# Kernel optimization log

Hardware: AMD Instinct MI355X
Metric: run time of the kernel (lower is better)

Reference implementation:

```python
import jax, jax.numpy as jnp
import numpy as np

B, T = 32, 1000
NN, NB, CTX = 512, 16, 64
EMB = 256
DCAT = 3 * EMB
H, L = 256, 4
PN, PB = 512, 2
S, V = 8, 64


def setup_inputs() -> dict:
    key = jax.random.key(0)
    ks = jax.random.split(key, 20)
    r = lambda i, shape, sc=1.0: jax.random.normal(ks[i], shape, dtype=jnp.float32) * sc
    nu_log = jnp.log(-jnp.log(jax.random.uniform(ks[8], (L, H), minval=0.5, maxval=0.95)))
    inp = {
        'neural_input': r(0, (B, T, NN)),
        'behavior_input': r(1, (B, T, NB)),
        'session_id': jax.random.randint(ks[2], (B,), 0, V),
        'subject_id': jax.random.randint(ks[3], (B,), 0, S),
        'session_table': r(4, (V, CTX), 0.02),
        'neural_W': r(5, (S, EMB, NN), 1.0 / np.sqrt(NN)),
        'neural_b': jnp.zeros((S, EMB), jnp.float32),
        'behavior_W': r(6, (S, EMB, NB), 1.0 / np.sqrt(NB)),
        'behavior_b': jnp.zeros((S, EMB), jnp.float32),
        'ctx_W': r(7, (EMB, CTX), 1.0 / np.sqrt(CTX)),
        'ctx_b': jnp.zeros((EMB,), jnp.float32),
        'nu_log': nu_log,
        'theta_log': jnp.log(jax.random.uniform(ks[9], (L, H), minval=1e-4, maxval=6.283)),
        'gamma_log': 0.5 * jnp.log1p(-jnp.exp(-2.0 * jnp.exp(nu_log))),
        'B_re': r(10, (L, H, DCAT), 1.0 / np.sqrt(2 * DCAT)),
        'B_im': r(11, (L, H, DCAT), 1.0 / np.sqrt(2 * DCAT)),
        'C_re': r(12, (L, DCAT, H), 1.0 / np.sqrt(H)),
        'C_im': r(13, (L, DCAT, H), 1.0 / np.sqrt(H)),
        'D_skip': r(14, (L, DCAT)),
        'dec_n_W': r(15, (S, PN, DCAT), 1.0 / np.sqrt(DCAT)),
        'dec_n_b': jnp.zeros((S, PN), jnp.float32),
        'dec_b_W': r(16, (S, PB, DCAT), 1.0 / np.sqrt(DCAT)),
        'dec_b_b': jnp.zeros((S, PB), jnp.float32),
    }
    return inp


def _lru(u, nu_log, theta_log, gamma_log, B_re, B_im, C_re, C_im, D_skip):
    # Linear Recurrent Unit: complex diagonal recurrence x_t = lam*x_{t-1} + gamma*B u_t
    lam = jnp.exp(-jnp.exp(nu_log) + 1j * jnp.exp(theta_log))  # [H]
    g = jnp.exp(gamma_log)[:, None]
    Bu = (jnp.einsum('bti,hi->bth', u, B_re * g)
          + 1j * jnp.einsum('bti,hi->bth', u, B_im * g))  # [B,T,H] complex

    def step(x, bu_t):
        x = lam * x + bu_t
        return x, x

    x0 = jnp.zeros((u.shape[0], nu_log.shape[0]), jnp.complex64)
    _, xs = jax.lax.scan(step, x0, jnp.swapaxes(Bu, 0, 1))
    xs = jnp.swapaxes(xs, 0, 1)  # [B,T,H]
    y = jnp.einsum('bth,oh->bto', xs, C_re + 1j * C_im).real + D_skip * u
    return y


def _forward(neural_input, behavior_input, session_table, neural_W, neural_b,
             behavior_W, behavior_b, ctx_W, ctx_b, nu_log, theta_log, gamma_log,
             B_re, B_im, C_re, C_im, D_skip, dec_n_W, dec_n_b, dec_b_W, dec_b_b,
             session_id, subject_id):
    act = jax.nn.relu
    Bsz, Ts, _ = neural_input.shape
    # session-token embedding -> context embedder (Linear is per-timestep, so embed once then broadcast)
    ctx = act(session_table[session_id] @ ctx_W.T + ctx_b)  # [B,EMB]
    ctx = jnp.broadcast_to(ctx[:, None, :], (Bsz, Ts, ctx.shape[-1]))
    # subject-routed embedders: gather per-sample weights, one batched GEMM
    en = act(jnp.einsum('btf,bef->bte', neural_input, neural_W[subject_id])
             + neural_b[subject_id][:, None, :])
    eb = act(jnp.einsum('btf,bef->bte', behavior_input, behavior_W[subject_id])
             + behavior_b[subject_id][:, None, :])
    h = jnp.concatenate([en, eb, ctx], axis=-1)  # [B,T,3*EMB]
    for l in range(nu_log.shape[0]):
        h = _lru(h, nu_log[l], theta_log[l], gamma_log[l],
                 B_re[l], B_im[l], C_re[l], C_im[l], D_skip[l])
    # subject-routed decoders
    pred_n = jax.nn.softplus(jnp.einsum('btd,bod->bto', h, dec_n_W[subject_id])
                             + dec_n_b[subject_id][:, None, :])
    pred_b = (jnp.einsum('btd,bod->bto', h, dec_b_W[subject_id])
              + dec_b_b[subject_id][:, None, :])
    return pred_n, pred_b


def reference(neural_input, behavior_input, session_id, subject_id, session_table,
              neural_W, neural_b, behavior_W, behavior_b, ctx_W, ctx_b,
              nu_log, theta_log, gamma_log, B_re, B_im, C_re, C_im, D_skip,
              dec_n_W, dec_n_b, dec_b_W, dec_b_b):
    return _forward(neural_input, behavior_input, session_table, neural_W, neural_b,
                    behavior_W, behavior_b, ctx_W, ctx_b, nu_log, theta_log, gamma_log,
                    B_re, B_im, C_re, C_im, D_skip, dec_n_W, dec_n_b, dec_b_W, dec_b_b,
                    session_id, subject_id)
```

## Files before the change

### kernel.cpp

```cpp
#include <hip/hip_runtime.h>

typedef __bf16 bf16;
typedef __bf16 bf16x8 __attribute__((ext_vector_type(8)));
typedef float f32x4 __attribute__((ext_vector_type(4)));

#define AS1 __attribute__((address_space(1)))
#define AS3 __attribute__((address_space(3)))

__device__ __forceinline__ void gll16(const void* g, void* l) {
    __builtin_amdgcn_global_load_lds((const AS1 void*)g, (AS3 void*)l, 16, 0, 0);
}

template<int EPI>
__global__ __launch_bounds__(512, 2)
void gemm_kern(const bf16* __restrict__ Abase, long long aBstride, int lda,
               const bf16* __restrict__ Wbase, long long wSstride,
               const float* __restrict__ biasBase, int biasStride,
               void* __restrict__ Cbase, long long cBstride, int ldc,
               const float* __restrict__ dskip,
               const bf16* __restrict__ Ubase, long long uBstride,
               const int* __restrict__ subj,
               int M, int K, int nbn)
{
    __shared__ char smem[147456];

    const int tid = threadIdx.x;
    const int lane = tid & 63;
    const int wid = tid >> 6;
    const int wm = wid >> 1, wn = wid & 1;
    const int l15 = lane & 15, lhi = lane >> 4;
    const int sw7 = l15 & 7;

    const int nwg = gridDim.x;
    const int bid = blockIdx.x;
    const int q = nwg >> 3, r = nwg & 7;
    const int xcd = bid & 7;
    const int sw = xcd * q + (xcd < r ? xcd : r) + (bid >> 3);
    const int m0 = (sw / nbn) * 256;
    const int n0 = (sw % nbn) * 128;

    const int b = blockIdx.z;
    const int s = subj ? subj[b] : 0;
    const bf16* A = Abase + (size_t)b * aBstride;
    const bf16* W = Wbase + (size_t)s * wSstride;
    const float* bias = biasBase ? biasBase + (size_t)s * biasStride : nullptr;
    const bf16* U = Ubase ? Ubase + (size_t)b * uBstride : nullptr;
    const size_t coff = (size_t)b * cBstride;
    const int Mc = M - 1;

    f32x4 acc[4][4];
    #pragma unroll
    for (int i = 0; i < 4; ++i)
        #pragma unroll
        for (int j = 0; j < 4; ++j)
            acc[i][j] = f32x4{0.f, 0.f, 0.f, 0.f};

    int rA[4], rB[4];
    #pragma unroll
    for (int f = 0; f < 4; ++f) {
        rA[f] = (wm*64 + f*16 + l15) * 128;
        rB[f] = (wn*64 + f*16 + l15) * 128;
    }

    const int sub  = tid >> 3;
    const int slot = tid & 7;
    const int ldsw = (wid << 10);

    auto stage = [&](int kt, char* buf) {
        #pragma unroll
        for (int c = 0; c < 4; ++c) {
            const int row = c*64 + sub;
            const int gk = (kt << 6) + ((slot ^ (row & 7)) << 3);
            int ar = m0 + row; if (ar > Mc) ar = Mc;
            gll16(A + (size_t)ar * lda + gk, buf + c*8192 + ldsw);
        }
        #pragma unroll
        for (int c = 0; c < 2; ++c) {
            const int row = c*64 + sub;
            const int gk = (kt << 6) + ((slot ^ (row & 7)) << 3);
            gll16(W + (size_t)(n0 + row) * K + gk, buf + 32768 + c*8192 + ldsw);
        }
    };

    char* cur = smem;
    char* nxt = smem + 49152;
    char* nn  = smem + 98304;

    const int nkt = K >> 6;
    stage(0, cur);
    if (nkt > 1) stage(1, nxt);
    asm volatile("s_waitcnt vmcnt(6)" ::: "memory");
    __builtin_amdgcn_s_barrier();

    for (int t = 0; t < nkt; ++t) {
        if (t + 2 < nkt) stage(t + 2, nn);

        #pragma unroll
        for (int kk = 0; kk < 2; ++kk) {
            const int so_ = (((kk << 2) | lhi) ^ sw7) << 4;
            bf16x8 af[4], bg[4];
            #pragma unroll
            for (int f = 0; f < 4; ++f) af[f] = *(const bf16x8*)(cur + rA[f] + so_);
            #pragma unroll
            for (int g = 0; g < 4; ++g) bg[g] = *(const bf16x8*)(cur + 32768 + rB[g] + so_);
            #pragma unroll
            for (int i = 0; i < 4; ++i)
                #pragma unroll
                for (int j = 0; j < 4; ++j)
                    acc[i][j] = __builtin_amdgcn_mfma_f32_16x16x32_bf16(
                        af[i], bg[j], acc[i][j], 0, 0, 0);
        }

        if (t + 2 < nkt) {
            asm volatile("s_waitcnt vmcnt(6)" ::: "memory");
        } else if (t + 1 < nkt) {
            asm volatile("s_waitcnt vmcnt(0)" ::: "memory");
        }
        if (t + 1 < nkt) __builtin_amdgcn_s_barrier();

        char* tmp = cur; cur = nxt; nxt = nn; nn = tmp;
    }

    __syncthreads();
    #pragma unroll
    for (int i = 0; i < 4; ++i) {
        #pragma unroll
        for (int j = 0; j < 4; ++j) {
            const int colb = (wn*64 + j*16 + l15) * 2;
            const f32x4 v = acc[i][j];
            #pragma unroll
            for (int qq = 0; qq < 4; ++qq) {
                const int row = wm*64 + i*16 + lhi*4 + qq;
                const int ad = row*256 + (colb & 15) + ((((colb >> 4) ^ (row & 7)) & 15) << 4);
                *(bf16*)(smem + ad) = (bf16)v[qq];
            }
        }
    }
    __syncthreads();

    #pragma unroll
    for (int u = 0; u < 8; ++u) {
        const int chunk = u*512 + tid;
        const int rr = chunk >> 4, ss = chunk & 15;
        const int gr = m0 + rr;
        if (gr >= M) continue;
        const int col = n0 + ss*8;
        const bf16x8 v = *(const bf16x8*)(smem + rr*256 + ((ss ^ (rr & 7)) << 4));
        if constexpr (EPI == 0) {
            const size_t ci = coff + (size_t)gr * ldc + col;
            *(bf16x8*)((bf16*)Cbase + ci) = v;
        } else if constexpr (EPI == 1) {
            const float4 b0 = *(const float4*)(bias + col);
            const float4 b1 = *(const float4*)(bias + col + 4);
            bf16x8 o;
            o[0] = (bf16)fmaxf((float)v[0] + b0.x, 0.f);
            o[1] = (bf16)fmaxf((float)v[1] + b0.y, 0.f);
            o[2] = (bf16)fmaxf((float)v[2] + b0.z, 0.f);
            o[3] = (bf16)fmaxf((float)v[3] + b0.w, 0.f);
            o[4] = (bf16)fmaxf((float)v[4] + b1.x, 0.f);
            o[5] = (bf16)fmaxf((float)v[5] + b1.y, 0.f);
            o[6] = (bf16)fmaxf((float)v[6] + b1.z, 0.f);
            o[7] = (bf16)fmaxf((float)v[7] + b1.w, 0.f);
            const size_t ci = coff + (size_t)gr * ldc + col;
            *(bf16x8*)((bf16*)Cbase + ci) = o;
        } else if constexpr (EPI == 2) {
            const bf16x8 uv = *(const bf16x8*)(U + (size_t)gr * ldc + col);
            const float4 d0 = *(const float4*)(dskip + col);
            const float4 d1 = *(const float4*)(dskip + col + 4);
            bf16x8 o;
            o[0] = (bf16)((float)v[0] + d0.x * (float)uv[0]);
            o[1] = (bf16)((float)v[1] + d0.y * (float)uv[1]);
            o[2] = (bf16)((float)v[2] + d0.z * (float)uv[2]);
            o[3] = (bf16)((float)v[3] + d0.w * (float)uv[3]);
            o[4] = (bf16)((float)v[4] + d1.x * (float)uv[4]);
            o[5] = (bf16)((float)v[5] + d1.y * (float)uv[5]);
            o[6] = (bf16)((float)v[6] + d1.z * (float)uv[6]);
            o[7] = (bf16)((float)v[7] + d1.w * (float)uv[7]);
            const size_t ci = coff + (size_t)gr * ldc + col;
            *(bf16x8*)((bf16*)Cbase + ci) = o;
        } else {
            const float4 b0 = *(const float4*)(bias + col);
            const float4 b1 = *(const float4*)(bias + col + 4);
            float xv[8];
            xv[0] = (float)v[0] + b0.x; xv[1] = (float)v[1] + b0.y;
            xv[2] = (float)v[2] + b0.z; xv[3] = (float)v[3] + b0.w;
            xv[4] = (float)v[4] + b1.x; xv[5] = (float)v[5] + b1.y;
            xv[6] = (float)v[6] + b1.z; xv[7] = (float)v[7] + b1.w;
            float4 o0, o1;
            #pragma unroll
            for (int e = 0; e < 8; ++e) {
                const float x = xv[e];
                const float sp = fmaxf(x, 0.f) + log1pf(expf(-fabsf(x)));
                if (e < 4) ((float*)&o0)[e] = sp; else ((float*)&o1)[e-4] = sp;
            }
            const size_t ci = coff + (size_t)gr * ldc + col;
            *(float4*)((float*)Cbase + ci) = o0;
            *(float4*)((float*)Cbase + ci + 4) = o1;
        }
    }
}

__global__ void scan_finals(const bf16* __restrict__ Bu,
                            const float* __restrict__ nu_log,
                            const float* __restrict__ theta_log,
                            float2* __restrict__ finals)
{
    const int g = blockIdx.x * 256 + threadIdx.x;
    const int h = g & 255;
    const int c = (g >> 8) % 20;
    const int b = g / 5120;
    const float a  = expf(nu_log[h]);
    const float th = expf(theta_log[h]);
    const float mag = expf(-a);
    const float lre = mag * cosf(th), lim = mag * sinf(th);
    float xre = 0.f, xim = 0.f;
    const bf16* p = Bu + ((size_t)(b*1000 + c*50)) * 512 + h;
    for (int i = 0; i < 50; ++i) {
        const float bre = (float)p[0], bim = (float)p[256];
        const float nre = lre*xre - lim*xim + bre;
        const float nim = lre*xim + lim*xre + bim;
        xre = nre; xim = nim;
        p += 512;
    }
    finals[(b*20 + c)*256 + h] = make_float2(xre, xim);
}

__global__ void scan_carry(const float2* __restrict__ finals,
                           float2* __restrict__ carry,
                           const float* __restrict__ nu_log,
                           const float* __restrict__ theta_log)
{
    const int g = blockIdx.x * 256 + threadIdx.x;
    const int h = g & 255;
    const int b = g >> 8;
    const float a  = expf(nu_log[h]);
    const float th = expf(theta_log[h]);
    const float mag = expf(-50.f * a);
    const float ang = 50.f * th;
    const float cre = mag * cosf(ang), cim = mag * sinf(ang);
    float pre = 0.f, pim = 0.f;
    for (int c = 0; c < 20; ++c) {
        const int idx = (b*20 + c)*256 + h;
        carry[idx] = make_float2(pre, pim);
        const float2 f = finals[idx];
        const float nre = f.x + cre*pre - cim*pim;
        const float nim = f.y + cre*pim + cim*pre;
        pre = nre; pim = nim;
    }
}

__global__ void scan_emit(const bf16* __restrict__ Bu,
                          const float2* __restrict__ carry,
                          const float* __restrict__ nu_log,
                          const float* __restrict__ theta_log,
                          bf16* __restrict__ xs)
{
    const int g = blockIdx.x * 256 + threadIdx.x;
    const int h = g & 255;
    const int c = (g >> 8) % 20;
    const int b = g / 5120;
    const float a  = expf(nu_log[h]);
    const float th = expf(theta_log[h]);
    const float mag = expf(-a);
    const float lre = mag * cosf(th), lim = mag * sinf(th);
    const float2 cr = carry[(b*20 + c)*256 + h];
    float xre = cr.x, xim = cr.y;
    const bf16* p = Bu + ((size_t)(b*1000 + c*50)) * 512 + h;
    bf16* qp = xs + ((size_t)(b*1000 + c*50)) * 512 + h;
    for (int i = 0; i < 50; ++i) {
        const float bre = (float)p[0], bim = (float)p[256];
        const float nre = lre*xre - lim*xim + bre;
        const float nim = lre*xim + lim*xre + bim;
        xre = nre; xim = nim;
        qp[0] = (bf16)xre; qp[256] = (bf16)xim;
        p += 512; qp += 512;
    }
}

__global__ void cast8_kern(const float* __restrict__ src, bf16* __restrict__ dst, int n8)
{
    const int i = blockIdx.x * 256 + threadIdx.x;
    if (i >= n8) return;
    const float4* s = (const float4*)src + (size_t)i*2;
    const float4 v0 = s[0], v1 = s[1];
    bf16x8 o;
    o[0] = (bf16)v0.x; o[1] = (bf16)v0.y; o[2] = (bf16)v0.z; o[3] = (bf16)v0.w;
    o[4] = (bf16)v1.x; o[5] = (bf16)v1.y; o[6] = (bf16)v1.z; o[7] = (bf16)v1.w;
    *((bf16x8*)dst + i) = o;
}

__global__ void packWB_kern(const float* __restrict__ Bre, const float* __restrict__ Bim,
                            const float* __restrict__ glog, bf16* __restrict__ WB)
{
    const int idx = blockIdx.x * 256 + threadIdx.x;
    if (idx >= 4*512*768) return;
    const int l = idx / (512*768);
    const int r = idx - l*(512*768);
    const int n = r / 768;
    const int k = r - n*768;
    float v;
    if (n < 256) v = Bre[((size_t)(l*256 + n))*768 + k] * expf(glog[l*256 + n]);
    else         v = Bim[((size_t)(l*256 + (n-256)))*768 + k] * expf(glog[l*256 + (n-256)]);
    WB[idx] = (bf16)v;
}

__global__ void packWC_kern(const float* __restrict__ Cre, const float* __restrict__ Cim,
                            bf16* __restrict__ WC)
{
    const int idx = blockIdx.x * 256 + threadIdx.x;
    if (idx >= 4*768*512) return;
    const int l = idx / (768*512);
    const int r = idx - l*(768*512);
    const int o = r / 512;
    const int k = r - o*512;
    const float v = (k < 256) ? Cre[((size_t)(l*768 + o))*256 + k]
                              : -Cim[((size_t)(l*768 + o))*256 + (k - 256)];
    WC[idx] = (bf16)v;
}

__global__ void ctx_kern(const float* __restrict__ st, const int* __restrict__ sess,
                         const float* __restrict__ cW, const float* __restrict__ cb,
                         float* __restrict__ ctx)
{
    const int b = blockIdx.x;
    const int e = threadIdx.x;
    const int sid = sess[b];
    const float* r = st + (size_t)sid * 64;
    const float* w = cW + (size_t)e * 64;
    float acc = cb[e];
    #pragma unroll 8
    for (int i = 0; i < 64; ++i) acc += r[i] * w[i];
    ctx[b*256 + e] = fmaxf(acc, 0.f);
}

__global__ void ebctx_kern(const float* __restrict__ behav,
                           const float* __restrict__ bW,
                           const float* __restrict__ bB,
                           const int* __restrict__ subj,
                           const float* __restrict__ ctx,
                           bf16* __restrict__ h0)
{
    const int blk = blockIdx.x;
    const int b = blk / 1000;
    const int e = threadIdx.x;
    __shared__ float binp[16];
    if (e < 16) binp[e] = behav[(size_t)blk*16 + e];
    __syncthreads();
    const int s = subj[b];
    const float* w = bW + ((size_t)(s*256) + e)*16;
    float acc = bB[s*256 + e];
    #pragma unroll
    for (int i = 0; i < 16; ++i) acc += binp[i] * w[i];
    acc = fmaxf(acc, 0.f);
    bf16* hp = h0 + (size_t)blk * 768;
    hp[256 + e] = (bf16)acc;
    hp[512 + e] = (bf16)ctx[b*256 + e];
}

__global__ void predb_kern(const bf16* __restrict__ h, const float* __restrict__ W,
                           const float* __restrict__ bb, const int* __restrict__ subj,
                           float* __restrict__ out)
{
    const int lane = threadIdx.x & 63;
    const int wid  = threadIdx.x >> 6;
    const int row  = blockIdx.x * 4 + wid;
    const int b = row / 1000;
    const int s = subj[b];
    const bf16* hr = h + (size_t)row * 768;
    const float* w0 = W + (size_t)(s*2) * 768;
    const float* w1 = w0 + 768;
    float a0 = 0.f, a1 = 0.f;
    #pragma unroll
    for (int j = 0; j < 12; ++j) {
        const int idx = j*64 + lane;
        const float hv = (float)hr[idx];
        a0 += hv * w0[idx];
        a1 += hv * w1[idx];
    }
    #pragma unroll
    for (int m = 32; m >= 1; m >>= 1) {
        a0 += __shfl_xor(a0, m);
        a1 += __shfl_xor(a1, m);
    }
    if (lane == 0) {
        out[(size_t)row*2 + 0] = a0 + bb[s*2 + 0];
        out[(size_t)row*2 + 1] = a1 + bb[s*2 + 1];
    }
}

extern "C" void kernel_launch(void* const* d_in, const int* in_sizes, int n_in,
                              void* d_out, int out_size, void* d_ws, size_t ws_size,
                              hipStream_t stream)
{
    const float* neural_input   = (const float*)d_in[0];
    const float* behavior_input = (const float*)d_in[1];
    const int*   session_id     = (const int*)d_in[2];
    const int*   subject_id     = (const int*)d_in[3];
    const float* session_table  = (const float*)d_in[4];
    const float* neural_W  = (const float*)d_in[5];
    const float* neural_b  = (const float*)d_in[6];
    const float* behavior_W = (const float*)d_in[7];
    const float* behavior_b = (const float*)d_in[8];
    const float* ctx_W = (const float*)d_in[9];
    const float* ctx_b = (const float*)d_in[10];
    const float* nu_log    = (const float*)d_in[11];
    const float* theta_log = (const float*)d_in[12];
    const float* gamma_log = (const float*)d_in[13];
    const float* B_re = (const float*)d_in[14];
    const float* B_im = (const float*)d_in[15];
    const float* C_re = (const float*)d_in[16];
    const float* C_im = (const float*)d_in[17];
    const float* D_skip = (const float*)d_in[18];
    const float* dec_n_W = (const float*)d_in[19];
    const float* dec_n_b = (const float*)d_in[20];
    const float* dec_b_W = (const float*)d_in[21];
    const float* dec_b_b = (const float*)d_in[22];
    float* out = (float*)d_out;

    char* ws = (char*)d_ws;
    size_t off = 0;
    auto alloc = [&](size_t bytes) -> char* {
        char* p = ws + off;
        off += (bytes + 255) & ~(size_t)255;
        return p;
    };
    bf16*   Wn      = (bf16*)alloc((size_t)8*256*512*2);
    bf16*   Wd      = (bf16*)alloc((size_t)8*512*768*2);
    bf16*   WB      = (bf16*)alloc((size_t)4*512*768*2);
    bf16*   WC      = (bf16*)alloc((size_t)4*768*512*2);
    float*  ctxbuf  = (float*)alloc((size_t)32*256*4);
    bf16*   hA      = (bf16*)alloc((size_t)32*1000*768*2);
    bf16*   hB      = (bf16*)alloc((size_t)32*1000*768*2);
    bf16*   xs      = (bf16*)alloc((size_t)32*1000*512*2);
    float2* finals  = (float2*)alloc((size_t)32*20*256*8);
    float2* carry   = (float2*)alloc((size_t)32*20*256*8);
    bf16*   Bu      = (bf16*)alloc((size_t)32*1000*512*2);
    bf16*   nbf     = Bu;

    cast8_kern<<<dim3(512),   256, 0, stream>>>(neural_W, Wn, 131072);
    cast8_kern<<<dim3(1536),  256, 0, stream>>>(dec_n_W,  Wd, 393216);
    packWB_kern<<<dim3(6144), 256, 0, stream>>>(B_re, B_im, gamma_log, WB);
    packWC_kern<<<dim3(6144), 256, 0, stream>>>(C_re, C_im, WC);
    ctx_kern<<<dim3(32), 256, 0, stream>>>(session_table, session_id, ctx_W, ctx_b, ctxbuf);
    cast8_kern<<<dim3(8000), 256, 0, stream>>>(neural_input, nbf, 2048000);

    ebctx_kern<<<dim3(32000), 256, 0, stream>>>(behavior_input, behavior_W, behavior_b,
                                                subject_id, ctxbuf, hA);
    gemm_kern<1><<<dim3(8, 1, 32), 512, 0, stream>>>(
        nbf, 512000LL, 512, Wn, 131072LL, neural_b, 256,
        hA, 768000LL, 768, nullptr, nullptr, 0LL, subject_id, 1000, 512, 2);

    for (int l = 0; l < 4; ++l) {
        const bf16* hin  = (l & 1) ? hB : hA;
        bf16*       hout = (l & 1) ? hA : hB;
        gemm_kern<0><<<dim3(500, 1, 1), 512, 0, stream>>>(
            hin, 0LL, 768, WB + (size_t)l*393216, 0LL, nullptr, 0,
            Bu, 0LL, 512, nullptr, nullptr, 0LL, nullptr, 32000, 768, 4);
        scan_finals<<<dim3(640), 256, 0, stream>>>(Bu, nu_log + l*256, theta_log + l*256, finals);
        scan_carry<<<dim3(32), 256, 0, stream>>>(finals, carry, nu_log + l*256, theta_log + l*256);
        scan_emit<<<dim3(640), 256, 0, stream>>>(Bu, carry, nu_log + l*256, theta_log + l*256, xs);
        gemm_kern<2><<<dim3(750, 1, 1), 512, 0, stream>>>(
            xs, 0LL, 512, WC + (size_t)l*393216, 0LL, nullptr, 0,
            hout, 0LL, 768, D_skip + l*768, hin, 0LL, nullptr, 32000, 512, 6);
    }

    gemm_kern<3><<<dim3(16, 1, 32), 512, 0, stream>>>(
        hA, 768000LL, 768, Wd, 393216LL, dec_n_b, 512,
        out, 512000LL, 512, nullptr, nullptr, 0LL, subject_id, 1000, 768, 4);
    predb_kern<<<dim3(8000), 256, 0, stream>>>(hA, dec_b_W, dec_b_b, subject_id,
                                               out + 16384000);
}
```

Measured before the change: 606.4 us.

## Shrink GEMM tile to 128x128 with 256 threads and K-step 32

The bf16 MFMA GEMM moves from a 256x128 tile with 8 waves and 64-wide K stages to a 128x128 tile with 4 waves and 32-wide K stages. The LDS XOR swizzle is reworked for 64-byte rows, and the next-stage prefetch is now issued after the MFMA block. LDS use drops from 144KB to 48KB and grids double, aiming for more resident workgroups and better latency hiding. In exchange, each output tile reloads A and W data more often, and there is more barrier overhead per unit of K.

Result: no change. 598.9 us (-1.2%).

```diff
diff --git a/kernel.cpp b/kernel.cpp
--- a/kernel.cpp
+++ b/kernel.cpp
@@ -12,7 +12,7 @@
 }
 
 template<int EPI>
-__global__ __launch_bounds__(512, 2)
+__global__ __launch_bounds__(256, 3)
 void gemm_kern(const bf16* __restrict__ Abase, long long aBstride, int lda,
                const bf16* __restrict__ Wbase, long long wSstride,
                const float* __restrict__ biasBase, int biasStride,
@@ -22,21 +22,21 @@
                const int* __restrict__ subj,
                int M, int K, int nbn)
 {
-    __shared__ char smem[147456];
+    __shared__ char smem[49152];
 
     const int tid = threadIdx.x;
     const int lane = tid & 63;
     const int wid = tid >> 6;
     const int wm = wid >> 1, wn = wid & 1;
     const int l15 = lane & 15, lhi = lane >> 4;
-    const int sw7 = l15 & 7;
+    const int sw3 = l15 & 3;
 
     const int nwg = gridDim.x;
     const int bid = blockIdx.x;
     const int q = nwg >> 3, r = nwg & 7;
     const int xcd = bid & 7;
     const int sw = xcd * q + (xcd < r ? xcd : r) + (bid >> 3);
-    const int m0 = (sw / nbn) * 256;
+    const int m0 = (sw / nbn) * 128;
     const int n0 = (sw % nbn) * 128;
 
     const int b = blockIdx.z;
@@ -58,67 +58,62 @@
     int rA[4], rB[4];
     #pragma unroll
     for (int f = 0; f < 4; ++f) {
-        rA[f] = (wm*64 + f*16 + l15) * 128;
-        rB[f] = (wn*64 + f*16 + l15) * 128;
-    }
-
-    const int sub  = tid >> 3;
-    const int slot = tid & 7;
+        rA[f] = (wm*64 + f*16 + l15) * 64;
+        rB[f] = (wn*64 + f*16 + l15) * 64;
+    }
+
+    const int sub  = tid >> 2;
+    const int slot = tid & 3;
     const int ldsw = (wid << 10);
 
-    auto stage = [&](int kt, char* buf) {
-        #pragma unroll
-        for (int c = 0; c < 4; ++c) {
-            const int row = c*64 + sub;
-            const int gk = (kt << 6) + ((slot ^ (row & 7)) << 3);
+    auto stage = [&](int kt, int bufo) {
+        #pragma unroll
+        for (int p = 0; p < 2; ++p) {
+            const int row = p*64 + sub;
+            const int gk = (kt << 5) + ((slot ^ (row & 3)) << 3);
             int ar = m0 + row; if (ar > Mc) ar = Mc;
-            gll16(A + (size_t)ar * lda + gk, buf + c*8192 + ldsw);
+            gll16(A + (size_t)ar * lda + gk, smem + bufo + p*4096 + ldsw);
         }
         #pragma unroll
-        for (int c = 0; c < 2; ++c) {
-            const int row = c*64 + sub;
-            const int gk = (kt << 6) + ((slot ^ (row & 7)) << 3);
-            gll16(W + (size_t)(n0 + row) * K + gk, buf + 32768 + c*8192 + ldsw);
+        for (int p = 0; p < 2; ++p) {
+            const int row = p*64 + sub;
+            const int gk = (kt << 5) + ((slot ^ (row & 3)) << 3);
+            gll16(W + (size_t)(n0 + row) * K + gk, smem + bufo + 8192 + p*4096 + ldsw);
         }
     };
 
-    char* cur = smem;
-    char* nxt = smem + 49152;
-    char* nn  = smem + 98304;
-
-    const int nkt = K >> 6;
-    stage(0, cur);
-    if (nkt > 1) stage(1, nxt);
-    asm volatile("s_waitcnt vmcnt(6)" ::: "memory");
+    const int nkt = K >> 5;
+    stage(0, 0);
+    stage(1, 16384);
+    asm volatile("s_waitcnt vmcnt(4)" ::: "memory");
     __builtin_amdgcn_s_barrier();
 
+    int curo = 0, nno = 32768;
     for (int t = 0; t < nkt; ++t) {
-        if (t + 2 < nkt) stage(t + 2, nn);
-
-        #pragma unroll
-        for (int kk = 0; kk < 2; ++kk) {
-            const int so_ = (((kk << 2) | lhi) ^ sw7) << 4;
-            bf16x8 af[4], bg[4];
+        const char* cb = smem + curo;
+        const int so_ = (lhi ^ sw3) << 4;
+        bf16x8 af[4], bg[4];
+        #pragma unroll
+        for (int f = 0; f < 4; ++f) af[f] = *(const bf16x8*)(cb + rA[f] + so_);
+        #pragma unroll
+        for (int g = 0; g < 4; ++g) bg[g] = *(const bf16x8*)(cb + 8192 + rB[g] + so_);
+        #pragma unroll
+        for (int i = 0; i < 4; ++i)
             #pragma unroll
-            for (int f = 0; f < 4; ++f) af[f] = *(const bf16x8*)(cur + rA[f] + so_);
-            #pragma unroll
-            for (int g = 0; g < 4; ++g) bg[g] = *(const bf16x8*)(cur + 32768 + rB[g] + so_);
-            #pragma unroll
-            for (int i = 0; i < 4; ++i)
-                #pragma unroll
-                for (int j = 0; j < 4; ++j)
-                    acc[i][j] = __builtin_amdgcn_mfma_f32_16x16x32_bf16(
-                        af[i], bg[j], acc[i][j], 0, 0, 0);
-        }
+            for (int j = 0; j < 4; ++j)
+                acc[i][j] = __builtin_amdgcn_mfma_f32_16x16x32_bf16(
+                    af[i], bg[j], acc[i][j], 0, 0, 0);
 
         if (t + 2 < nkt) {
-            asm volatile("s_waitcnt vmcnt(6)" ::: "memory");
+            stage(t + 2, nno);
+            asm volatile("s_waitcnt vmcnt(4)" ::: "memory");
+            __builtin_amdgcn_s_barrier();
         } else if (t + 1 < nkt) {
             asm volatile("s_waitcnt vmcnt(0)" ::: "memory");
+            __builtin_amdgcn_s_barrier();
         }
-        if (t + 1 < nkt) __builtin_amdgcn_s_barrier();
-
-        char* tmp = cur; cur = nxt; nxt = nn; nn = tmp;
+        curo += 16384; if (curo == 49152) curo = 0;
+        nno  += 16384; if (nno  == 49152) nno  = 0;
     }
 
     __syncthreads();
@@ -140,7 +135,7 @@
 
     #pragma unroll
     for (int u = 0; u < 8; ++u) {
-        const int chunk = u*512 + tid;
+        const int chunk = u*256 + tid;
         const int rr = chunk >> 4, ss = chunk & 15;
         const int gr = m0 + rr;
         if (gr >= M) continue;
@@ -446,25 +441,25 @@
 
     ebctx_kern<<<dim3(32000), 256, 0, stream>>>(behavior_input, behavior_W, behavior_b,
                                                 subject_id, ctxbuf, hA);
-    gemm_kern<1><<<dim3(8, 1, 32), 512, 0, stream>>>(
+    gemm_kern<1><<<dim3(16, 1, 32), 256, 0, stream>>>(
         nbf, 512000LL, 512, Wn, 131072LL, neural_b, 256,
         hA, 768000LL, 768, nullptr, nullptr, 0LL, subject_id, 1000, 512, 2);
 
     for (int l = 0; l < 4; ++l) {
         const bf16* hin  = (l & 1) ? hB : hA;
         bf16*       hout = (l & 1) ? hA : hB;
-        gemm_kern<0><<<dim3(500, 1, 1), 512, 0, stream>>>(
+        gemm_kern<0><<<dim3(1000, 1, 1), 256, 0, stream>>>(
             hin, 0LL, 768, WB + (size_t)l*393216, 0LL, nullptr, 0,
             Bu, 0LL, 512, nullptr, nullptr, 0LL, nullptr, 32000, 768, 4);
         scan_finals<<<dim3(640), 256, 0, stream>>>(Bu, nu_log + l*256, theta_log + l*256, finals);
         scan_carry<<<dim3(32), 256, 0, stream>>>(finals, carry, nu_log + l*256, theta_log + l*256);
         scan_emit<<<dim3(640), 256, 0, stream>>>(Bu, carry, nu_log + l*256, theta_log + l*256, xs);
-        gemm_kern<2><<<dim3(750, 1, 1), 512, 0, stream>>>(
+        gemm_kern<2><<<dim3(1500, 1, 1), 256, 0, stream>>>(
             xs, 0LL, 512, WC + (size_t)l*393216, 0LL, nullptr, 0,
             hout, 0LL, 768, D_skip + l*768, hin, 0LL, nullptr, 32000, 512, 6);
     }
 
-    gemm_kern<3><<<dim3(16, 1, 32), 512, 0, stream>>>(
+    gemm_kern<3><<<dim3(32, 1, 32), 256, 0, stream>>>(
         hA, 768000LL, 768, Wd, 393216LL, dec_n_b, 512,
         out, 512000LL, 512, nullptr, nullptr, 0LL, subject_id, 1000, 768, 4);
     predb_kern<<<dim3(8000), 256, 0, stream>>>(hA, dec_b_W, dec_b_b, subject_id,
```

## Interleave GEMM loads with MFMA clusters via barriers and priority; batch ebctx over timesteps

Applied to the files above, without the earlier changes.

The GEMM main loop becomes four explicitly scheduled phases. In each phase a few LDS fragment reads and global-to-LDS prefetches are issued, followed by a barrier, an lgkmcnt wait, and a raised-priority cluster of 8 MFMAs, so memory traffic overlaps with matrix math. The launch bound drops from 2 to 1 block per CU, and the 147KB of shared memory already limited occupancy. Separately, the behavior/context embedding kernel now loads its weights into registers once and loops over 125 timesteps per block, going from 32000 tiny blocks to 256. The many added barriers could cost more than the overlap gains, and with only 256 blocks the embedding kernel may underuse the GPU.

Result: slower. 620.6 us (+2.3%).

```diff
diff --git a/kernel.cpp b/kernel.cpp
--- a/kernel.cpp
+++ b/kernel.cpp
@@ -11,8 +11,13 @@
     __builtin_amdgcn_global_load_lds((const AS1 void*)g, (AS3 void*)l, 16, 0, 0);
 }
 
+#define BAR()      __builtin_amdgcn_s_barrier()
+#define LGKM0()    do { asm volatile("s_waitcnt lgkmcnt(0)" ::: "memory"); \
+                        __builtin_amdgcn_sched_barrier(0); } while (0)
+#define PRIO(x)    __builtin_amdgcn_s_setprio(x)
+
 template<int EPI>
-__global__ __launch_bounds__(512, 2)
+__global__ __launch_bounds__(512, 1)
 void gemm_kern(const bf16* __restrict__ Abase, long long aBstride, int lda,
                const bf16* __restrict__ Wbase, long long wSstride,
                const float* __restrict__ biasBase, int biasStride,
@@ -59,66 +64,108 @@
     #pragma unroll
     for (int f = 0; f < 4; ++f) {
         rA[f] = (wm*64 + f*16 + l15) * 128;
-        rB[f] = (wn*64 + f*16 + l15) * 128;
-    }
+        rB[f] = 32768 + (wn*64 + f*16 + l15) * 128;
+    }
+    const int so0 = ((lhi       ^ sw7) << 4);
+    const int so1 = (((4 | lhi) ^ sw7) << 4);
 
     const int sub  = tid >> 3;
     const int slot = tid & 7;
     const int ldsw = (wid << 10);
-
-    auto stage = [&](int kt, char* buf) {
-        #pragma unroll
-        for (int c = 0; c < 4; ++c) {
-            const int row = c*64 + sub;
-            const int gk = (kt << 6) + ((slot ^ (row & 7)) << 3);
-            int ar = m0 + row; if (ar > Mc) ar = Mc;
-            gll16(A + (size_t)ar * lda + gk, buf + c*8192 + ldsw);
-        }
-        #pragma unroll
-        for (int c = 0; c < 2; ++c) {
-            const int row = c*64 + sub;
-            const int gk = (kt << 6) + ((slot ^ (row & 7)) << 3);
-            gll16(W + (size_t)(n0 + row) * K + gk, buf + 32768 + c*8192 + ldsw);
-        }
+    const int swk  = (slot ^ (sub & 7)) << 3;
+
+    auto stA = [&](int kt, int bufo, int c) {
+        const int row = c*64 + sub;
+        int ar = m0 + row; if (ar > Mc) ar = Mc;
+        gll16(A + (size_t)ar * lda + (kt << 6) + swk, smem + bufo + c*8192 + ldsw);
     };
-
-    char* cur = smem;
-    char* nxt = smem + 49152;
-    char* nn  = smem + 98304;
+    auto stB = [&](int kt, int bufo, int c) {
+        gll16(W + (size_t)(n0 + c*64 + sub) * K + (kt << 6) + swk,
+              smem + bufo + 32768 + c*8192 + ldsw);
+    };
 
     const int nkt = K >> 6;
-    stage(0, cur);
-    if (nkt > 1) stage(1, nxt);
+    stA(0, 0, 0); stA(0, 0, 1); stA(0, 0, 2); stA(0, 0, 3);
+    stB(0, 0, 0); stB(0, 0, 1);
+    stA(1, 49152, 0); stA(1, 49152, 1); stA(1, 49152, 2); stA(1, 49152, 3);
+    stB(1, 49152, 0); stB(1, 49152, 1);
     asm volatile("s_waitcnt vmcnt(6)" ::: "memory");
-    __builtin_amdgcn_s_barrier();
-
+    BAR();
+
+    int curo = 0, nno = 98304;
     for (int t = 0; t < nkt; ++t) {
-        if (t + 2 < nkt) stage(t + 2, nn);
-
-        #pragma unroll
-        for (int kk = 0; kk < 2; ++kk) {
-            const int so_ = (((kk << 2) | lhi) ^ sw7) << 4;
-            bf16x8 af[4], bg[4];
-            #pragma unroll
-            for (int f = 0; f < 4; ++f) af[f] = *(const bf16x8*)(cur + rA[f] + so_);
-            #pragma unroll
-            for (int g = 0; g < 4; ++g) bg[g] = *(const bf16x8*)(cur + 32768 + rB[g] + so_);
-            #pragma unroll
-            for (int i = 0; i < 4; ++i)
-                #pragma unroll
-                for (int j = 0; j < 4; ++j)
-                    acc[i][j] = __builtin_amdgcn_mfma_f32_16x16x32_bf16(
-                        af[i], bg[j], acc[i][j], 0, 0, 0);
-        }
-
-        if (t + 2 < nkt) {
-            asm volatile("s_waitcnt vmcnt(6)" ::: "memory");
-        } else if (t + 1 < nkt) {
-            asm volatile("s_waitcnt vmcnt(0)" ::: "memory");
-        }
-        if (t + 1 < nkt) __builtin_amdgcn_s_barrier();
-
-        char* tmp = cur; cur = nxt; nxt = nn; nn = tmp;
+        const char* cb = smem + curo;
+        const bool st = (t + 2 < nkt);
+        bf16x8 a0, a1, a2, a3, b0, b1, b2, b3;
+
+        a0 = *(const bf16x8*)(cb + rA[0] + so0);
+        a1 = *(const bf16x8*)(cb + rA[1] + so0);
+        b0 = *(const bf16x8*)(cb + rB[0] + so0);
+        b1 = *(const bf16x8*)(cb + rB[1] + so0);
+        b2 = *(const bf16x8*)(cb + rB[2] + so0);
+        b3 = *(const bf16x8*)(cb + rB[3] + so0);
+        if (st) { stA(t + 2, nno, 0); stA(t + 2, nno, 1); }
+        BAR(); LGKM0(); PRIO(1);
+        acc[0][0] = __builtin_amdgcn_mfma_f32_16x16x32_bf16(a0, b0, acc[0][0], 0, 0, 0);
+        acc[0][1] = __builtin_amdgcn_mfma_f32_16x16x32_bf16(a0, b1, acc[0][1], 0, 0, 0);
+        acc[0][2] = __builtin_amdgcn_mfma_f32_16x16x32_bf16(a0, b2, acc[0][2], 0, 0, 0);
+        acc[0][3] = __builtin_amdgcn_mfma_f32_16x16x32_bf16(a0, b3, acc[0][3], 0, 0, 0);
+        acc[1][0] = __builtin_amdgcn_mfma_f32_16x16x32_bf16(a1, b0, acc[1][0], 0, 0, 0);
+        acc[1][1] = __builtin_amdgcn_mfma_f32_16x16x32_bf16(a1, b1, acc[1][1], 0, 0, 0);
+        acc[1][2] = __builtin_amdgcn_mfma_f32_16x16x32_bf16(a1, b2, acc[1][2], 0, 0, 0);
+        acc[1][3] = __builtin_amdgcn_mfma_f32_16x16x32_bf16(a1, b3, acc[1][3], 0, 0, 0);
+        PRIO(0); BAR();
+
+        a2 = *(const bf16x8*)(cb + rA[2] + so0);
+        a3 = *(const bf16x8*)(cb + rA[3] + so0);
+        if (st) { stA(t + 2, nno, 2); stA(t + 2, nno, 3); }
+        BAR(); LGKM0(); PRIO(1);
+        acc[2][0] = __builtin_amdgcn_mfma_f32_16x16x32_bf16(a2, b0, acc[2][0], 0, 0, 0);
+        acc[2][1] = __builtin_amdgcn_mfma_f32_16x16x32_bf16(a2, b1, acc[2][1], 0, 0, 0);
+        acc[2][2] = __builtin_amdgcn_mfma_f32_16x16x32_bf16(a2, b2, acc[2][2], 0, 0, 0);
+        acc[2][3] = __builtin_amdgcn_mfma_f32_16x16x32_bf16(a2, b3, acc[2][3], 0, 0, 0);
+        acc[3][0] = __builtin_amdgcn_mfma_f32_16x16x32_bf16(a3, b0, acc[3][0], 0, 0, 0);
+        acc[3][1] = __builtin_amdgcn_mfma_f32_16x16x32_bf16(a3, b1, acc[3][1], 0, 0, 0);
+        acc[3][2] = __builtin_amdgcn_mfma_f32_16x16x32_bf16(a3, b2, acc[3][2], 0, 0, 0);
+        acc[3][3] = __builtin_amdgcn_mfma_f32_16x16x32_bf16(a3, b3, acc[3][3], 0, 0, 0);
+        PRIO(0); BAR();
+
+        a0 = *(const bf16x8*)(cb + rA[0] + so1);
+        a1 = *(const bf16x8*)(cb + rA[1] + so1);
+        b0 = *(const bf16x8*)(cb + rB[0] + so1);
+        b1 = *(const bf16x8*)(cb + rB[1] + so1);
+        b2 = *(const bf16x8*)(cb + rB[2] + so1);
+        b3 = *(const bf16x8*)(cb + rB[3] + so1);
+        if (st) { stB(t + 2, nno, 0); stB(t + 2, nno, 1); }
+        BAR(); LGKM0(); PRIO(1);
+        acc[0][0] = __builtin_amdgcn_mfma_f32_16x16x32_bf16(a0, b0, acc[0][0], 0, 0, 0);
+        acc[0][1] = __builtin_amdgcn_mfma_f32_16x16x32_bf16(a0, b1, acc[0][1], 0, 0, 0);
+        acc[0][2] = __builtin_amdgcn_mfma_f32_16x16x32_bf16(a0, b2, acc[0][2], 0, 0, 0);
+        acc[0][3] = __builtin_amdgcn_mfma_f32_16x16x32_bf16(a0, b3, acc[0][3], 0, 0, 0);
+        acc[1][0] = __builtin_amdgcn_mfma_f32_16x16x32_bf16(a1, b0, acc[1][0], 0, 0, 0);
+        acc[1][1] = __builtin_amdgcn_mfma_f32_16x16x32_bf16(a1, b1, acc[1][1], 0, 0, 0);
+        acc[1][2] = __builtin_amdgcn_mfma_f32_16x16x32_bf16(a1, b2, acc[1][2], 0, 0, 0);
+        acc[1][3] = __builtin_amdgcn_mfma_f32_16x16x32_bf16(a1, b3, acc[1][3], 0, 0, 0);
+        PRIO(0); BAR();
+
+        a2 = *(const bf16x8*)(cb + rA[2] + so1);
+        a3 = *(const bf16x8*)(cb + rA[3] + so1);
+        BAR(); LGKM0(); PRIO(1);
+        acc[2][0] = __builtin_amdgcn_mfma_f32_16x16x32_bf16(a2, b0, acc[2][0], 0, 0, 0);
+        acc[2][1] = __builtin_amdgcn_mfma_f32_16x16x32_bf16(a2, b1, acc[2][1], 0, 0, 0);
+        acc[2][2] = __builtin_amdgcn_mfma_f32_16x16x32_bf16(a2, b2, acc[2][2], 0, 0, 0);
+        acc[2][3] = __builtin_amdgcn_mfma_f32_16x16x32_bf16(a2, b3, acc[2][3], 0, 0, 0);
+        acc[3][0] = __builtin_amdgcn_mfma_f32_16x16x32_bf16(a3, b0, acc[3][0], 0, 0, 0);
+        acc[3][1] = __builtin_amdgcn_mfma_f32_16x16x32_bf16(a3, b1, acc[3][1], 0, 0, 0);
+        acc[3][2] = __builtin_amdgcn_mfma_f32_16x16x32_bf16(a3, b2, acc[3][2], 0, 0, 0);
+        acc[3][3] = __builtin_amdgcn_mfma_f32_16x16x32_bf16(a3, b3, acc[3][3], 0, 0, 0);
+        PRIO(0);
+        if (st)               { asm volatile("s_waitcnt vmcnt(6)" ::: "memory"); }
+        else if (t + 1 < nkt) { asm volatile("s_waitcnt vmcnt(0)" ::: "memory"); }
+        BAR();
+
+        curo = (curo == 98304) ? 0 : curo + 49152;
+        nno  = (nno  == 98304) ? 0 : nno  + 49152;
     }
 
     __syncthreads();
@@ -340,21 +387,27 @@
                            const float* __restrict__ ctx,
                            bf16* __restrict__ h0)
 {
-    const int blk = blockIdx.x;
-    const int b = blk / 1000;
+    const int b  = blockIdx.x >> 3;
+    const int tc = blockIdx.x & 7;
     const int e = threadIdx.x;
-    __shared__ float binp[16];
-    if (e < 16) binp[e] = behav[(size_t)blk*16 + e];
-    __syncthreads();
     const int s = subj[b];
+    float wreg[16];
     const float* w = bW + ((size_t)(s*256) + e)*16;
-    float acc = bB[s*256 + e];
-    #pragma unroll
-    for (int i = 0; i < 16; ++i) acc += binp[i] * w[i];
-    acc = fmaxf(acc, 0.f);
-    bf16* hp = h0 + (size_t)blk * 768;
-    hp[256 + e] = (bf16)acc;
-    hp[512 + e] = (bf16)ctx[b*256 + e];
+    #pragma unroll
+    for (int i = 0; i < 16; ++i) wreg[i] = w[i];
+    const float bb_ = bB[s*256 + e];
+    const bf16 cx = (bf16)ctx[b*256 + e];
+    const int t0 = tc * 125;
+    for (int t = t0; t < t0 + 125; ++t) {
+        const int blk = b*1000 + t;
+        const float* bi = behav + (size_t)blk * 16;
+        float acc = bb_;
+        #pragma unroll
+        for (int i = 0; i < 16; ++i) acc += bi[i] * wreg[i];
+        bf16* hp = h0 + (size_t)blk * 768;
+        hp[256 + e] = (bf16)fmaxf(acc, 0.f);
+        hp[512 + e] = cx;
+    }
 }
 
 __global__ void predb_kern(const bf16* __restrict__ h, const float* __restrict__ W,
@@ -444,8 +497,8 @@
     ctx_kern<<<dim3(32), 256, 0, stream>>>(session_table, session_id, ctx_W, ctx_b, ctxbuf);
     cast8_kern<<<dim3(8000), 256, 0, stream>>>(neural_input, nbf, 2048000);
 
-    ebctx_kern<<<dim3(32000), 256, 0, stream>>>(behavior_input, behavior_W, behavior_b,
-                                                subject_id, ctxbuf, hA);
+    ebctx_kern<<<dim3(256), 256, 0, stream>>>(behavior_input, behavior_W, behavior_b,
+                                              subject_id, ctxbuf, hA);
     gemm_kern<1><<<dim3(8, 1, 32), 512, 0, stream>>>(
         nbf, 512000LL, 512, Wn, 131072LL, neural_b, 256,
         hA, 768000LL, 768, nullptr, nullptr, 0LL, subject_id, 1000, 512, 2);
```
